# Kernel tuning notes

Hardware: AMD Instinct MI355X
Metric: run time of the kernel (lower is better)

## Reference

```python
import jax, jax.numpy as jnp
import numpy as np

B, S, H, NH = 2, 2048, 1024, 16
DH = H // NH
FF = 4 * H
EPS = 1e-5


def setup_inputs() -> dict:
    key = jax.random.key(0)
    ks = jax.random.split(key, 16)
    sd = 0.02
    inp = {
        "x": jax.random.normal(ks[0], (B, S, H), dtype=jnp.float32),
        "Wq": jax.random.normal(ks[1], (H, H), dtype=jnp.float32) * sd,
        "bq": jnp.zeros((H,), jnp.float32),
        "Wk": jax.random.normal(ks[2], (H, H), dtype=jnp.float32) * sd,
        "bk": jnp.zeros((H,), jnp.float32),
        "Wv": jax.random.normal(ks[3], (H, H), dtype=jnp.float32) * sd,
        "bv": jnp.zeros((H,), jnp.float32),
        "Wo": jax.random.normal(ks[4], (H, H), dtype=jnp.float32) * sd,
        "bo": jnp.zeros((H,), jnp.float32),
        "W1": jax.random.normal(ks[5], (H, FF), dtype=jnp.float32) * sd,
        "b1": jnp.zeros((FF,), jnp.float32),
        "W2": jax.random.normal(ks[6], (FF, H), dtype=jnp.float32) * sd,
        "b2": jnp.zeros((H,), jnp.float32),
        "g1": jnp.ones((H,), jnp.float32),
        "be1": jnp.zeros((H,), jnp.float32),
        "g2": jnp.ones((H,), jnp.float32),
        "be2": jnp.zeros((H,), jnp.float32),
    }
    return inp


def _layernorm(x, g, b):
    mu = jnp.mean(x, axis=-1, keepdims=True)
    var = jnp.mean(jnp.square(x - mu), axis=-1, keepdims=True)
    return (x - mu) * jax.lax.rsqrt(var + EPS) * g + b


def _block(x, Wq, bq, Wk, bk, Wv, bv, Wo, bo, W1, b1, W2, b2, g1, be1, g2, be2):
    # pre-LN attention
    h = _layernorm(x, g1, be1)
    q = (h @ Wq + bq).reshape(B, S, NH, DH)
    k = (h @ Wk + bk).reshape(B, S, NH, DH)
    v = (h @ Wv + bv).reshape(B, S, NH, DH)
    scale = DH ** -0.5
    scores = jnp.einsum("bqhd,bkhd->bhqk", q, k) * scale  # [B,NH,S,S]
    causal = jnp.tril(jnp.ones((S, S), dtype=bool))
    scores = jnp.where(causal, scores, -jnp.inf)
    attn = jax.nn.softmax(scores, axis=-1)
    out = jnp.einsum("bhqk,bkhd->bqhd", attn, v).reshape(B, S, H)
    x = x + (out @ Wo + bo)
    # pre-LN FFN with exact GELU (torch nn.GELU default)
    h = _layernorm(x, g2, be2)
    h = jax.nn.gelu(h @ W1 + b1, approximate=False)
    return x + (h @ W2 + b2)


def reference(x, Wq, bq, Wk, bk, Wv, bv, Wo, bo, W1, b1, W2, b2, g1, be1, g2, be2):
    return _block(x, Wq, bq, Wk, bk, Wv, bv, Wo, bo, W1, b1, W2, b2, g1, be1, g2, be2)
```

## Files before the change

### kernel.cpp

```cpp
#include <hip/hip_runtime.h>
#include <cstdint>
#include <cstddef>

typedef unsigned short u16;
typedef __attribute__((ext_vector_type(8))) __bf16 bf16v8;
typedef __attribute__((ext_vector_type(8))) unsigned short u16x8;
typedef __attribute__((ext_vector_type(4))) float f32x4;

constexpr int Bc = 2, Sc = 2048, Hc = 1024, NHc = 16, DHc = 64, FFc = 4096;
constexpr int Mc = Bc * Sc;

__device__ __forceinline__ u16 f2bf(float f) {
  unsigned u = __builtin_bit_cast(unsigned, f);
  return (u16)((u + 0x7FFFu + ((u >> 16) & 1u)) >> 16);
}

__device__ __forceinline__ int xcd_swz(int bid, int n) {
  const int q = n >> 3;
  return (bid & 7) * q + (bid >> 3);
}

__device__ __forceinline__ void gload_lds16(const void* g, void* l) {
  __builtin_amdgcn_global_load_lds(
      (const __attribute__((address_space(1))) unsigned*)(uintptr_t)g,
      (__attribute__((address_space(3))) unsigned*)(unsigned)(uintptr_t)l,
      16, 0, 0);
}

struct WP4 { const float* w0; const float* w1; const float* w2; const float* w3; };
__global__ __launch_bounds__(256) void wconv4_kernel(WP4 p, u16* __restrict__ Wt) {
  __shared__ float tile[64][65];
  const float* W = (blockIdx.z == 0) ? p.w0 : (blockIdx.z == 1) ? p.w1
                  : (blockIdx.z == 2) ? p.w2 : p.w3;
  u16* dst = Wt + (size_t)blockIdx.z * 1024 * 1024;
  const int n0 = blockIdx.x << 6, k0 = blockIdx.y << 6;
  const int t = threadIdx.x;
  const int col = t & 63, r0 = t >> 6;
#pragma unroll
  for (int i = 0; i < 16; ++i) {
    int r = (i << 2) + r0;
    tile[r][col] = W[(size_t)(k0 + r) * 1024 + n0 + col];
  }
  __syncthreads();
#pragma unroll
  for (int i = 0; i < 16; ++i) {
    int n = (i << 2) + r0;
    dst[(size_t)(n0 + n) * 1024 + k0 + col] = f2bf(tile[col][n]);
  }
}

__global__ __launch_bounds__(256) void wconv_kernel(const float* __restrict__ W,
                                                    u16* __restrict__ Wt, int K, int N) {
  __shared__ float tile[64][65];
  const int n0 = blockIdx.x << 6, k0 = blockIdx.y << 6;
  const int t = threadIdx.x;
  const int col = t & 63, r0 = t >> 6;
#pragma unroll
  for (int i = 0; i < 16; ++i) {
    int r = (i << 2) + r0;
    tile[r][col] = W[(size_t)(k0 + r) * N + n0 + col];
  }
  __syncthreads();
#pragma unroll
  for (int i = 0; i < 16; ++i) {
    int n = (i << 2) + r0;
    Wt[(size_t)(n0 + n) * K + k0 + col] = f2bf(tile[col][n]);
  }
}

__global__ __launch_bounds__(256) void ln_kernel(const float* __restrict__ x,
                                                 const float* __restrict__ g,
                                                 const float* __restrict__ be,
                                                 u16* __restrict__ y) {
  const int row = blockIdx.x;
  const int t = threadIdx.x;
  const float4 v = ((const float4*)(x + (size_t)row * Hc))[t];
  float s1 = v.x + v.y + v.z + v.w;
  float s2 = v.x * v.x + v.y * v.y + v.z * v.z + v.w * v.w;
#pragma unroll
  for (int o = 32; o > 0; o >>= 1) {
    s1 += __shfl_xor(s1, o);
    s2 += __shfl_xor(s2, o);
  }
  __shared__ float r1[4], r2[4];
  const int wave = t >> 6, lane = t & 63;
  if (lane == 0) { r1[wave] = s1; r2[wave] = s2; }
  __syncthreads();
  s1 = r1[0] + r1[1] + r1[2] + r1[3];
  s2 = r2[0] + r2[1] + r2[2] + r2[3];
  const float mu = s1 * (1.f / Hc);
  const float var = s2 * (1.f / Hc) - mu * mu;
  const float rs = rsqrtf(var + 1e-5f);
  const float4 gv = ((const float4*)g)[t];
  const float4 bv = ((const float4*)be)[t];
  ushort4 ov;
  ov.x = f2bf((v.x - mu) * rs * gv.x + bv.x);
  ov.y = f2bf((v.y - mu) * rs * gv.y + bv.y);
  ov.z = f2bf((v.z - mu) * rs * gv.z + bv.z);
  ov.w = f2bf((v.w - mu) * rs * gv.w + bv.w);
  ((ushort4*)(y + (size_t)row * Hc))[t] = ov;
}

template <int EPI>
__global__ __launch_bounds__(256, 2) void gemm_kernel(
    const u16* __restrict__ A, const u16* __restrict__ Bt,
    const float* __restrict__ bias, const float* __restrict__ res,
    u16* __restrict__ outb, float* __restrict__ outf, float* __restrict__ outf2,
    int N, int Kext, int lda, int ldb, int koff, int nx) {
  __shared__ __align__(16) char smraw[32768];
  u16 (*As)[128][32] = (u16(*)[128][32])smraw;
  u16 (*Bs)[128][32] = (u16(*)[128][32])(smraw + 16384);
  float (*Cs)[16][132] = (float(*)[16][132])smraw;

  const int t = threadIdx.x;
  const int wave = t >> 6, lane = t & 63;
  const int pid = xcd_swz(blockIdx.x, gridDim.x);
  const int bn = pid % nx, bm = pid / nx;
  const int kz = blockIdx.z;
  A += (size_t)kz * koff;
  Bt += (size_t)kz * koff;
  const int wm = wave >> 1, wn = wave & 1;
  const int fr = lane & 15, fk = (lane >> 4) << 3;

  f32x4 acc[4][4] = {};

  const int srow = (wave << 4) + (lane >> 2);
  const int scol = (lane & 3) << 3;
  const u16* Ag0 = A + (size_t)(bm * 128 + srow) * lda + scol;
  const u16* Ag1 = Ag0 + (size_t)64 * lda;
  const u16* Bg0 = Bt + (size_t)(bn * 128 + srow) * ldb + scol;
  const u16* Bg1 = Bg0 + (size_t)64 * ldb;

  const int nk = Kext >> 5;
  auto STAGE = [&](int buf, int k0) {
    gload_lds16(Ag0 + k0, &As[buf][wave << 4][0]);
    gload_lds16(Ag1 + k0, &As[buf][64 + (wave << 4)][0]);
    gload_lds16(Bg0 + k0, &Bs[buf][wave << 4][0]);
    gload_lds16(Bg1 + k0, &Bs[buf][64 + (wave << 4)][0]);
  };

  STAGE(0, 0);
  asm volatile("s_waitcnt vmcnt(0)" ::: "memory");
  __syncthreads();
  int cur = 0;
  for (int kt = 0; kt < nk; ++kt) {
    if (kt + 1 < nk) STAGE(cur ^ 1, (kt + 1) << 5);
    bf16v8 af[4], bfr[4];
#pragma unroll
    for (int i = 0; i < 4; ++i) af[i] = *(const bf16v8*)&As[cur][(wm << 6) + (i << 4) + fr][fk];
#pragma unroll
    for (int j = 0; j < 4; ++j) bfr[j] = *(const bf16v8*)&Bs[cur][(wn << 6) + (j << 4) + fr][fk];
    __builtin_amdgcn_s_setprio(1);
#pragma unroll
    for (int i = 0; i < 4; ++i)
#pragma unroll
      for (int j = 0; j < 4; ++j)
        acc[i][j] = __builtin_amdgcn_mfma_f32_16x16x32_bf16(af[i], bfr[j], acc[i][j], 0, 0, 0);
    __builtin_amdgcn_s_setprio(0);
    asm volatile("s_waitcnt vmcnt(0)" ::: "memory");
    __syncthreads();
    cur ^= 1;
  }

  const int cr = (lane >> 4) << 2, cc = lane & 15;
  const int b2 = t >> 7, u = t & 127, lr = u >> 3, c0 = (u & 7) << 4;
  float* fdst = (EPI == 3 && kz) ? outf2 : outf;

  for (int i = 0; i < 4; ++i) {
#pragma unroll
    for (int j = 0; j < 4; ++j) {
      int col = (wn << 6) + (j << 4) + cc;
      float bz = 0.f;
      if constexpr (EPI != 3) bz = bias[(bn << 7) + col];
#pragma unroll
      for (int r = 0; r < 4; ++r) Cs[wm][cr + r][col] = acc[i][j][r] + bz;
    }
    __syncthreads();
    {
      const float* crow = &Cs[b2][lr][c0];
      f32x4 v0 = *(const f32x4*)(crow);
      f32x4 v1 = *(const f32x4*)(crow + 4);
      f32x4 v2 = *(const f32x4*)(crow + 8);
      f32x4 v3 = *(const f32x4*)(crow + 12);
      const int grow = (bm << 7) + (b2 << 6) + (i << 4) + lr;
      const int gc = (bn << 7) + c0;
      const size_t base = (size_t)grow * N + gc;
      if constexpr (EPI == 0 || EPI == 1) {
        float vv[16];
#pragma unroll
        for (int k = 0; k < 4; ++k) { vv[k] = v0[k]; vv[4 + k] = v1[k]; vv[8 + k] = v2[k]; vv[12 + k] = v3[k]; }
        if constexpr (EPI == 1) {
#pragma unroll
          for (int k = 0; k < 16; ++k)
            vv[k] = 0.5f * vv[k] * (1.0f + erff(vv[k] * 0.70710678118654752f));
        }
        u16x8 o0, o1;
#pragma unroll
        for (int k = 0; k < 8; ++k) { o0[k] = f2bf(vv[k]); o1[k] = f2bf(vv[8 + k]); }
        *(u16x8*)&outb[base] = o0;
        *(u16x8*)&outb[base + 8] = o1;
      } else {
        if constexpr (EPI == 2) {
          const f32x4* rp = (const f32x4*)&res[base];
          v0 += rp[0]; v1 += rp[1]; v2 += rp[2]; v3 += rp[3];
        }
        f32x4* op = (f32x4*)&fdst[base];
        op[0] = v0; op[1] = v1; op[2] = v2; op[3] = v3;
      }
    }
    __syncthreads();
  }
}

__global__ __launch_bounds__(256, 2) void qkv_gemm_kernel(
    const u16* __restrict__ A, const u16* __restrict__ Bt,
    const float* __restrict__ bq, const float* __restrict__ bk,
    const float* __restrict__ bv,
    u16* __restrict__ Qb, u16* __restrict__ Kb, u16* __restrict__ Vtg) {
  constexpr int K = 1024;
  __shared__ __align__(16) char smraw[32768];
  u16 (*As)[128][32] = (u16(*)[128][32])smraw;
  u16 (*Bs)[128][32] = (u16(*)[128][32])(smraw + 16384);
  float (*Cs)[16][132] = (float(*)[16][132])smraw;

  const int t = threadIdx.x;
  const int wave = t >> 6, lane = t & 63;
  const int pid = xcd_swz(blockIdx.x, 768);
  const int bn = pid % 24, bm = pid / 24;
  const int wm = wave >> 1, wn = wave & 1;
  const int fr = lane & 15, fk = (lane >> 4) << 3;
  const int seg = bn >> 3;

  f32x4 acc[4][4] = {};

  const int srow = (wave << 4) + (lane >> 2);
  const int scol = (lane & 3) << 3;
  const u16* Ag0 = A + (size_t)(bm * 128 + srow) * K + scol;
  const u16* Ag1 = Ag0 + (size_t)64 * K;
  const u16* Bg0 = Bt + (size_t)(bn * 128 + srow) * K + scol;
  const u16* Bg1 = Bg0 + (size_t)64 * K;

  const int nk = K >> 5;
  auto STAGE = [&](int buf, int k0) {
    gload_lds16(Ag0 + k0, &As[buf][wave << 4][0]);
    gload_lds16(Ag1 + k0, &As[buf][64 + (wave << 4)][0]);
    gload_lds16(Bg0 + k0, &Bs[buf][wave << 4][0]);
    gload_lds16(Bg1 + k0, &Bs[buf][64 + (wave << 4)][0]);
  };

  STAGE(0, 0);
  asm volatile("s_waitcnt vmcnt(0)" ::: "memory");
  __syncthreads();
  int cur = 0;
  for (int kt = 0; kt < nk; ++kt) {
    if (kt + 1 < nk) STAGE(cur ^ 1, (kt + 1) << 5);
    bf16v8 af[4], bfr[4];
#pragma unroll
    for (int i = 0; i < 4; ++i) af[i] = *(const bf16v8*)&As[cur][(wm << 6) + (i << 4) + fr][fk];
#pragma unroll
    for (int j = 0; j < 4; ++j) bfr[j] = *(const bf16v8*)&Bs[cur][(wn << 6) + (j << 4) + fr][fk];
    __builtin_amdgcn_s_setprio(1);
#pragma unroll
    for (int i = 0; i < 4; ++i)
#pragma unroll
      for (int j = 0; j < 4; ++j)
        acc[i][j] = __builtin_amdgcn_mfma_f32_16x16x32_bf16(af[i], bfr[j], acc[i][j], 0, 0, 0);
    __builtin_amdgcn_s_setprio(0);
    asm volatile("s_waitcnt vmcnt(0)" ::: "memory");
    __syncthreads();
    cur ^= 1;
  }

  const int cr = (lane >> 4) << 2, cc = lane & 15;
  const int b2 = t >> 7, u = t & 127, lr = u >> 3, c0 = (u & 7) << 4;
  const float* bp = (seg == 0) ? bq : (seg == 1) ? bk : bv;

  for (int i = 0; i < 4; ++i) {
#pragma unroll
    for (int j = 0; j < 4; ++j) {
      int col = (wn << 6) + (j << 4) + cc;
      float bz = bp[((bn << 7) + col) & 1023];
#pragma unroll
      for (int r = 0; r < 4; ++r) Cs[wm][cr + r][col] = acc[i][j][r] + bz;
    }
    __syncthreads();
    if (seg < 2) {
      const float* crow = &Cs[b2][lr][c0];
      f32x4 v0 = *(const f32x4*)(crow);
      f32x4 v1 = *(const f32x4*)(crow + 4);
      f32x4 v2 = *(const f32x4*)(crow + 8);
      f32x4 v3 = *(const f32x4*)(crow + 12);
      const int grow = (bm << 7) + (b2 << 6) + (i << 4) + lr;
      const int cn0 = (((bn & 7) << 7) + c0);
      u16* dst = (seg == 0) ? Qb : Kb;
      u16x8 o0, o1;
#pragma unroll
      for (int k = 0; k < 4; ++k) {
        o0[k] = f2bf(v0[k]); o0[4 + k] = f2bf(v1[k]);
        o1[k] = f2bf(v2[k]); o1[4 + k] = f2bf(v3[k]);
      }
      *(u16x8*)&dst[(size_t)grow * 1024 + cn0] = o0;
      *(u16x8*)&dst[(size_t)grow * 1024 + cn0 + 8] = o1;
    } else {
      const int cv = ((bn & 7) << 7) + u;
      const int h = cv >> 6, dh = cv & 63;
#pragma unroll
      for (int oct = 0; oct < 2; ++oct) {
        u16x8 o;
#pragma unroll
        for (int k = 0; k < 8; ++k) o[k] = f2bf(Cs[b2][(oct << 3) + k][u]);
        const int srow2 = (bm << 7) + (b2 << 6) + (i << 4) + (oct << 3);
        const int bb = srow2 >> 11, s = srow2 & 2047;
        size_t idx = ((size_t)(bb * 16 + h)) * (64 * 2048) + (size_t)dh * 2048 + s;
        *(u16x8*)&Vtg[idx] = o;
      }
    }
    __syncthreads();
  }
}

__global__ __launch_bounds__(256) void combine_kernel(float* __restrict__ out,
                                                      const float* __restrict__ p0,
                                                      const float* __restrict__ p1,
                                                      const float* __restrict__ bias) {
  const int i = blockIdx.x * 256 + threadIdx.x;
  f32x4 o = ((f32x4*)out)[i];
  f32x4 a = ((const f32x4*)p0)[i];
  f32x4 b = ((const f32x4*)p1)[i];
  const int col = (i << 2) & 1023;
  f32x4 bb = *(const f32x4*)&bias[col];
  o += a + b + bb;
  ((f32x4*)out)[i] = o;
}

__global__ __launch_bounds__(256, 3) void attn_kernel(const u16* __restrict__ Q,
                                                      const u16* __restrict__ Kb,
                                                      const u16* __restrict__ Vt,
                                                      u16* __restrict__ O) {
  constexpr float CS = 0.18033688011112042f;
  constexpr float M2 = 8.0f;
  const int pid = xcd_swz(blockIdx.x, 512);
  const int bx = pid & 15, bh = pid >> 4;
  const int t = threadIdx.x, wave = t >> 6, lane = t & 63;
  const int fr = lane & 15, fk = (lane >> 4) << 3;

  __shared__ u16 Ks[2][64][72];
  __shared__ u16 Vs[2][64][72];
  __shared__ u16 Ps[4][16][72];

  const size_t base = ((size_t)(bh >> 4) * Sc) * Hc + (bh & 15) * DHc;
  const u16* Qp = Q + base;
  const u16* Kp = Kb + base;
  const u16* Vp = Vt + (size_t)bh * (64 * 2048);

  const int r_st = t >> 3;
  const int co_st = (t & 7) << 3;

  bf16v8 ones;
#pragma unroll
  for (int k = 0; k < 8; ++k) ones[k] = (__bf16)1.0f;

  for (int half = 0; half < 2; ++half) {
    const int qt = half ? (31 - bx) : bx;
    const int q0 = qt << 6;
    const int nt = qt + 1;

    const int qrow = q0 + (wave << 4) + fr;
    const bf16v8 qf0 = *(const bf16v8*)&Qp[(size_t)qrow * Hc + fk];
    const bf16v8 qf1 = *(const bf16v8*)&Qp[(size_t)qrow * Hc + 32 + fk];

    f32x4 oacc[4] = {};
    f32x4 osum = {};

    const int crow0 = q0 + (wave << 4) + ((lane >> 4) << 2);

    u16x8 rk0, rk1, rv0, rv1;
    auto LD = [&](int kv0) {
      rk0 = *(const u16x8*)&Kp[(size_t)(kv0 + r_st) * Hc + co_st];
      rk1 = *(const u16x8*)&Kp[(size_t)(kv0 + 32 + r_st) * Hc + co_st];
      rv0 = *(const u16x8*)&Vp[(size_t)r_st * 2048 + kv0 + co_st];
      rv1 = *(const u16x8*)&Vp[(size_t)(32 + r_st) * 2048 + kv0 + co_st];
    };
    auto WR = [&](int buf) {
      *(u16x8*)&Ks[buf][r_st][co_st] = rk0;
      *(u16x8*)&Ks[buf][32 + r_st][co_st] = rk1;
      *(u16x8*)&Vs[buf][r_st][co_st] = rv0;
      *(u16x8*)&Vs[buf][32 + r_st][co_st] = rv1;
    };

    LD(0);
    WR(0);
    __syncthreads();
    int cur = 0;
    for (int it = 0; it < nt; ++it) {
      const int kv0 = it << 6;
      const bool hasnext = (it + 1 < nt);
      if (hasnext) LD(kv0 + 64);

      f32x4 sc[4];
      __builtin_amdgcn_s_setprio(1);
#pragma unroll
      for (int c = 0; c < 4; ++c) {
        bf16v8 kf0 = *(const bf16v8*)&Ks[cur][(c << 4) + fr][fk];
        bf16v8 kf1 = *(const bf16v8*)&Ks[cur][(c << 4) + fr][32 + fk];
        f32x4 a = {0.f, 0.f, 0.f, 0.f};
        a = __builtin_amdgcn_mfma_f32_16x16x32_bf16(qf0, kf0, a, 0, 0, 0);
        a = __builtin_amdgcn_mfma_f32_16x16x32_bf16(qf1, kf1, a, 0, 0, 0);
        sc[c] = a;
      }
      __builtin_amdgcn_s_setprio(0);

      if (kv0 + 64 > q0) {
#pragma unroll
        for (int c = 0; c < 4; ++c)
#pragma unroll
          for (int r = 0; r < 4; ++r) {
            int kv = kv0 + (c << 4) + fr;
            if (kv > crow0 + r) sc[c][r] = -INFINITY;
          }
      }

#pragma unroll
      for (int c = 0; c < 4; ++c)
#pragma unroll
        for (int r = 0; r < 4; ++r) {
          float p = exp2f(fmaf(sc[c][r], CS, -M2));
          Ps[wave][((lane >> 4) << 2) + r][(c << 4) + fr] = f2bf(p);
        }

      const bf16v8 pa0 = *(const bf16v8*)&Ps[wave][fr][fk];
      const bf16v8 pa1 = *(const bf16v8*)&Ps[wave][fr][32 + fk];
      __builtin_amdgcn_s_setprio(1);
#pragma unroll
      for (int f = 0; f < 4; ++f) {
        bf16v8 vf0 = *(const bf16v8*)&Vs[cur][(f << 4) + fr][fk];
        bf16v8 vf1 = *(const bf16v8*)&Vs[cur][(f << 4) + fr][32 + fk];
        oacc[f] = __builtin_amdgcn_mfma_f32_16x16x32_bf16(pa0, vf0, oacc[f], 0, 0, 0);
        oacc[f] = __builtin_amdgcn_mfma_f32_16x16x32_bf16(pa1, vf1, oacc[f], 0, 0, 0);
      }
      osum = __builtin_amdgcn_mfma_f32_16x16x32_bf16(pa0, ones, osum, 0, 0, 0);
      osum = __builtin_amdgcn_mfma_f32_16x16x32_bf16(pa1, ones, osum, 0, 0, 0);
      __builtin_amdgcn_s_setprio(0);

      if (hasnext) WR(cur ^ 1);
      __syncthreads();
      cur ^= 1;
    }
#pragma unroll
    for (int r = 0; r < 4; ++r) {
      float inv = 1.0f / osum[r];
      int row = crow0 + r;
#pragma unroll
      for (int f = 0; f < 4; ++f)
        O[base + (size_t)row * Hc + (f << 4) + fr] = f2bf(oacc[f][r] * inv);
    }
    __syncthreads();
  }
}

extern "C" void kernel_launch(void* const* d_in, const int* in_sizes, int n_in,
                              void* d_out, int out_size, void* d_ws, size_t ws_size,
                              hipStream_t stream) {
  const float* x  = (const float*)d_in[0];
  const float* Wq = (const float*)d_in[1];
  const float* bq = (const float*)d_in[2];
  const float* Wk = (const float*)d_in[3];
  const float* bk = (const float*)d_in[4];
  const float* Wv = (const float*)d_in[5];
  const float* bv = (const float*)d_in[6];
  const float* Wo = (const float*)d_in[7];
  const float* bo = (const float*)d_in[8];
  const float* W1 = (const float*)d_in[9];
  const float* b1 = (const float*)d_in[10];
  const float* W2 = (const float*)d_in[11];
  const float* b2 = (const float*)d_in[12];
  const float* g1 = (const float*)d_in[13];
  const float* be1 = (const float*)d_in[14];
  const float* g2 = (const float*)d_in[15];
  const float* be2 = (const float*)d_in[16];
  float* out = (float*)d_out;

  char* ws = (char*)d_ws;
  const size_t MB = 1024 * 1024;
  u16* wqkv = (u16*)(ws + 0 * MB);
  u16* wo   = (u16*)(ws + 6 * MB);
  u16* w1   = (u16*)(ws + 8 * MB);
  u16* w2   = (u16*)(ws + 16 * MB);
  u16* lnb  = (u16*)(ws + 24 * MB);
  u16* Qb   = (u16*)(ws + 32 * MB);
  u16* Kb   = (u16*)(ws + 40 * MB);
  u16* Vtg  = (u16*)(ws + 48 * MB);
  u16* Ob   = (u16*)(ws + 56 * MB);
  u16* H1   = (u16*)(ws + 32 * MB);
  float* p0 = (float*)(ws + 64 * MB);
  float* p1 = (float*)(ws + 0 * MB);

  dim3 blk(256);
  WP4 wp{Wq, Wk, Wv, Wo};
  wconv4_kernel<<<dim3(16, 16, 4), blk, 0, stream>>>(wp, wqkv);
  wconv_kernel<<<dim3(64, 16), blk, 0, stream>>>(W1, w1, 1024, 4096);
  wconv_kernel<<<dim3(16, 64), blk, 0, stream>>>(W2, w2, 4096, 1024);

  ln_kernel<<<Mc, blk, 0, stream>>>(x, g1, be1, lnb);

  qkv_gemm_kernel<<<dim3(768), blk, 0, stream>>>(lnb, wqkv, bq, bk, bv, Qb, Kb, Vtg);

  attn_kernel<<<dim3(512), blk, 0, stream>>>(Qb, Kb, Vtg, Ob);

  gemm_kernel<2><<<dim3(256), blk, 0, stream>>>(Ob, wo, bo, x, nullptr, out, nullptr,
                                                1024, 1024, 1024, 1024, 0, 8);

  ln_kernel<<<Mc, blk, 0, stream>>>(out, g2, be2, lnb);

  gemm_kernel<1><<<dim3(1024), blk, 0, stream>>>(lnb, w1, b1, nullptr, H1, nullptr, nullptr,
                                                 4096, 1024, 1024, 1024, 0, 32);

  gemm_kernel<3><<<dim3(256, 1, 2), blk, 0, stream>>>(H1, w2, nullptr, nullptr, nullptr, p0, p1,
                                                      1024, 2048, 4096, 4096, 2048, 8);
  combine_kernel<<<dim3(4096), blk, 0, stream>>>(out, p0, p1, b2);
}
```

Before: 251.6 us.

## Triple-buffer GEMM LDS staging with partial vmcnt waits

Both the generic GEMM and the QKV GEMM move from double to triple buffering of the A/B tiles in LDS. Loads are issued two K-steps ahead, and the kernel waits only for the oldest stage via vmcnt counts instead of draining all loads every iteration. This lets global-to-LDS transfers overlap with MFMA work across more iterations. In exchange LDS per block grows from 32 KB to 48 KB, which may limit occupancy, and each iteration now has two raw barriers that depend on the correctness of the vmcnt counts.

```diff
diff --git a/kernel.cpp b/kernel.cpp
--- a/kernel.cpp
+++ b/kernel.cpp
@@ -107,9 +107,9 @@
     const float* __restrict__ bias, const float* __restrict__ res,
     u16* __restrict__ outb, float* __restrict__ outf, float* __restrict__ outf2,
     int N, int Kext, int lda, int ldb, int koff, int nx) {
-  __shared__ __align__(16) char smraw[32768];
+  __shared__ __align__(16) char smraw[49152];
   u16 (*As)[128][32] = (u16(*)[128][32])smraw;
-  u16 (*Bs)[128][32] = (u16(*)[128][32])(smraw + 16384);
+  u16 (*Bs)[128][32] = (u16(*)[128][32])(smraw + 24576);
   float (*Cs)[16][132] = (float(*)[16][132])smraw;
 
   const int t = threadIdx.x;
@@ -140,16 +140,26 @@
   };
 
   STAGE(0, 0);
-  asm volatile("s_waitcnt vmcnt(0)" ::: "memory");
-  __syncthreads();
+  STAGE(1, 32);
   int cur = 0;
   for (int kt = 0; kt < nk; ++kt) {
-    if (kt + 1 < nk) STAGE(cur ^ 1, (kt + 1) << 5);
+    if (kt + 2 < nk) {
+      int sb = cur + 2; if (sb >= 3) sb -= 3;
+      STAGE(sb, (kt + 2) << 5);
+      asm volatile("s_waitcnt vmcnt(8)" ::: "memory");
+    } else if (kt + 1 < nk) {
+      asm volatile("s_waitcnt vmcnt(4)" ::: "memory");
+    } else {
+      asm volatile("s_waitcnt vmcnt(0)" ::: "memory");
+    }
+    __builtin_amdgcn_s_barrier();
     bf16v8 af[4], bfr[4];
 #pragma unroll
     for (int i = 0; i < 4; ++i) af[i] = *(const bf16v8*)&As[cur][(wm << 6) + (i << 4) + fr][fk];
 #pragma unroll
     for (int j = 0; j < 4; ++j) bfr[j] = *(const bf16v8*)&Bs[cur][(wn << 6) + (j << 4) + fr][fk];
+    asm volatile("s_waitcnt lgkmcnt(0)" ::: "memory");
+    __builtin_amdgcn_s_barrier();
     __builtin_amdgcn_s_setprio(1);
 #pragma unroll
     for (int i = 0; i < 4; ++i)
@@ -157,10 +167,9 @@
       for (int j = 0; j < 4; ++j)
         acc[i][j] = __builtin_amdgcn_mfma_f32_16x16x32_bf16(af[i], bfr[j], acc[i][j], 0, 0, 0);
     __builtin_amdgcn_s_setprio(0);
-    asm volatile("s_waitcnt vmcnt(0)" ::: "memory");
-    __syncthreads();
-    cur ^= 1;
-  }
+    cur = (cur + 1 == 3) ? 0 : cur + 1;
+  }
+  __syncthreads();
 
   const int cr = (lane >> 4) << 2, cc = lane & 15;
   const int b2 = t >> 7, u = t & 127, lr = u >> 3, c0 = (u & 7) << 4;
@@ -218,9 +227,9 @@
     const float* __restrict__ bv,
     u16* __restrict__ Qb, u16* __restrict__ Kb, u16* __restrict__ Vtg) {
   constexpr int K = 1024;
-  __shared__ __align__(16) char smraw[32768];
+  __shared__ __align__(16) char smraw[49152];
   u16 (*As)[128][32] = (u16(*)[128][32])smraw;
-  u16 (*Bs)[128][32] = (u16(*)[128][32])(smraw + 16384);
+  u16 (*Bs)[128][32] = (u16(*)[128][32])(smraw + 24576);
   float (*Cs)[16][132] = (float(*)[16][132])smraw;
 
   const int t = threadIdx.x;
@@ -249,16 +258,26 @@
   };
 
   STAGE(0, 0);
-  asm volatile("s_waitcnt vmcnt(0)" ::: "memory");
-  __syncthreads();
+  STAGE(1, 32);
   int cur = 0;
   for (int kt = 0; kt < nk; ++kt) {
-    if (kt + 1 < nk) STAGE(cur ^ 1, (kt + 1) << 5);
+    if (kt + 2 < nk) {
+      int sb = cur + 2; if (sb >= 3) sb -= 3;
+      STAGE(sb, (kt + 2) << 5);
+      asm volatile("s_waitcnt vmcnt(8)" ::: "memory");
+    } else if (kt + 1 < nk) {
+      asm volatile("s_waitcnt vmcnt(4)" ::: "memory");
+    } else {
+      asm volatile("s_waitcnt vmcnt(0)" ::: "memory");
+    }
+    __builtin_amdgcn_s_barrier();
     bf16v8 af[4], bfr[4];
 #pragma unroll
     for (int i = 0; i < 4; ++i) af[i] = *(const bf16v8*)&As[cur][(wm << 6) + (i << 4) + fr][fk];
 #pragma unroll
     for (int j = 0; j < 4; ++j) bfr[j] = *(const bf16v8*)&Bs[cur][(wn << 6) + (j << 4) + fr][fk];
+    asm volatile("s_waitcnt lgkmcnt(0)" ::: "memory");
+    __builtin_amdgcn_s_barrier();
     __builtin_amdgcn_s_setprio(1);
 #pragma unroll
     for (int i = 0; i < 4; ++i)
@@ -266,10 +285,9 @@
       for (int j = 0; j < 4; ++j)
         acc[i][j] = __builtin_amdgcn_mfma_f32_16x16x32_bf16(af[i], bfr[j], acc[i][j], 0, 0, 0);
     __builtin_amdgcn_s_setprio(0);
-    asm volatile("s_waitcnt vmcnt(0)" ::: "memory");
-    __syncthreads();
-    cur ^= 1;
-  }
+    cur = (cur + 1 == 3) ? 0 : cur + 1;
+  }
+  __syncthreads();
 
   const int cr = (lane >> 4) << 2, cc = lane & 15;
   const int b2 = t >> 7, u = t & 127, lr = u >> 3, c0 = (u & 7) << 4;
```

Measured after the change: 252.2 us. Within noise of the previous version (+0.2%).
